# Performance work log

Measured on AMD Instinct MI355X. Metric: run time of the kernel, lower is better.

Reference implementation:

```python
import jax, jax.numpy as jnp
import numpy as np

HIDDEN = 1024

def setup_inputs() -> dict:
    key = jax.random.key(0)
    ks = jax.random.split(key, 7)
    B, S, H = 4, 4096, HIDDEN
    x = jax.random.normal(ks[0], (B, S, H), dtype=jnp.float32)
    s = 1.0 / np.sqrt(H)
    Wq = jax.random.normal(ks[1], (H, H), dtype=jnp.float32) * s
    bq = jnp.zeros((H,), dtype=jnp.float32)
    Wk = jax.random.normal(ks[2], (H, H), dtype=jnp.float32) * s
    bk = jnp.zeros((H,), dtype=jnp.float32)
    Wv = jax.random.normal(ks[3], (H, H), dtype=jnp.float32) * s
    bv = jnp.zeros((H,), dtype=jnp.float32)
    return {"x": x, "Wq": Wq, "bq": bq, "Wk": Wk, "bk": bk, "Wv": Wv, "bv": bv}

def reference(x, Wq, bq, Wk, bk, Wv, bv):
    # x: [B, S, H]
    scale = jnp.sqrt(jnp.asarray(x.shape[-1], dtype=x.dtype))
    q = jnp.einsum('bsh,hd->bsd', x, Wq) + bq
    k = jnp.einsum('bsh,hd->bsd', x, Wk) + bk
    v = jnp.einsum('bsh,hd->bsd', x, Wv) + bv
    energy = jnp.einsum('bqd,bkd->bqk', q, k) / scale  # [B, S, S]
    attn = jax.nn.softmax(energy, axis=-1)
    return jnp.einsum('bqk,bkd->bqd', attn, v)
```

## Files before the change

### kernel.cpp

```cpp
#include <hip/hip_runtime.h>

typedef unsigned short u16;
typedef __attribute__((ext_vector_type(8))) short short8;
typedef __attribute__((ext_vector_type(4))) short short4v;
typedef __attribute__((ext_vector_type(4))) float floatx4;

#define HD 1024
#define SEQ 4096

__device__ inline u16 f2bf(float f) {
    union { float f; unsigned int i; } c; c.f = f;
    unsigned int r = c.i + 0x7fffu + ((c.i >> 16) & 1u);
    return (u16)(r >> 16);
}

__device__ inline float bf2f(u16 h) {
    union { unsigned int u; float f; } c; c.u = ((unsigned int)h) << 16;
    return c.f;
}

__device__ inline int xcd_chunk(int bid, int nwg) {
    int q = nwg >> 3;
    return (bid & 7) * q + (bid >> 3);
}

__device__ inline void glds16(const u16* g, u16* l) {
    __builtin_amdgcn_global_load_lds(
        (const __attribute__((address_space(1))) unsigned int*)(const void*)g,
        (__attribute__((address_space(3))) unsigned int*)(void*)l, 16, 0, 0);
}

__global__ __launch_bounds__(256) void cvt_kernel(const float* __restrict__ in,
                                                  u16* __restrict__ out, int n4) {
    int idx = blockIdx.x * 256 + threadIdx.x;
    int stride = gridDim.x * 256;
    for (int i = idx; i < n4; i += stride) {
        floatx4 v = ((const floatx4*)in)[i];
        short4v o;
        o[0] = (short)f2bf(v[0]); o[1] = (short)f2bf(v[1]);
        o[2] = (short)f2bf(v[2]); o[3] = (short)f2bf(v[3]);
        ((short4v*)out)[i] = o;
    }
}

__global__ __launch_bounds__(256) void wt_kernel(const float* __restrict__ Wq,
                                                 const float* __restrict__ Wk,
                                                 const float* __restrict__ Wv,
                                                 u16* __restrict__ wt) {
    __shared__ u16 tile[64 * 65];
    int z = blockIdx.z;
    const float* W = (z == 0) ? Wq : ((z == 1) ? Wk : Wv);
    u16* out = wt + (size_t)z * HD * HD;
    int k0 = blockIdx.x * 64, n0 = blockIdx.y * 64;
    int t = threadIdx.x;
    int r = t >> 4, c4 = (t & 15) * 4;
    for (int h = 0; h < 4; ++h) {
        int row = r + h * 16;
        floatx4 v = *(const floatx4*)(W + (size_t)(k0 + row) * HD + n0 + c4);
        tile[row * 65 + c4 + 0] = f2bf(v[0]);
        tile[row * 65 + c4 + 1] = f2bf(v[1]);
        tile[row * 65 + c4 + 2] = f2bf(v[2]);
        tile[row * 65 + c4 + 3] = f2bf(v[3]);
    }
    __syncthreads();
    int r2 = t >> 3, c8 = (t & 7) * 8;
    union { short8 v; u16 u[8]; } buf;
    for (int h = 0; h < 2; ++h) {
        int rr = r2 + h * 32;
        #pragma unroll
        for (int i = 0; i < 8; ++i) buf.u[i] = tile[(c8 + i) * 65 + rr];
        *(short8*)(out + (size_t)(n0 + rr) * HD + k0 + c8) = buf.v;
    }
}

#define RD_A(i, ks) (*(const short8*)&As[(wm * 128 + (i) * 16 + l16) * 64 + ((((ks) * 4 + quad)) ^ (l16 & 7)) * 8])
#define RD_B(j, ks) (*(const short8*)&Bs[(wn * 64 + (j) * 16 + l16) * 64 + ((((ks) * 4 + quad)) ^ (l16 & 7)) * 8])

#define GEMM256_CORE(KTN, LDA_, LDB_)                                                   \
    int t = threadIdx.x, lane = t & 63, w = t >> 6;                                     \
    int quad = lane >> 4, l16 = lane & 15;                                              \
    int wm = w >> 2, wn = w & 3;                                                        \
    int l8r = lane >> 3;                                                                \
    int sswz = (lane & 7) ^ l8r;                                                        \
    const u16* gAs = Ab + (size_t)(m0 + w * 32 + l8r) * LDA_ + sswz * 8;                \
    const u16* gBs = Bb + (size_t)(n0 + w * 32 + l8r) * LDB_ + sswz * 8;                \
    auto stage = [&](int kt_) {                                                         \
        int s_ = kt_ & 1;                                                               \
        const u16* a0 = gAs + (size_t)kt_ * 64;                                         \
        const u16* b0 = gBs + (size_t)kt_ * 64;                                         \
        _Pragma("unroll")                                                               \
        for (int L = 0; L < 4; ++L) {                                                   \
            glds16(a0 + (size_t)(8 * L) * LDA_, &ring[s_][0][(w * 32 + 8 * L) * 64]);   \
            glds16(b0 + (size_t)(8 * L) * LDB_, &ring[s_][1][(w * 32 + 8 * L) * 64]);   \
        }                                                                               \
    };                                                                                  \
    floatx4 acc[8][4] = {};                                                             \
    stage(0);                                                                           \
    for (int kt = 0; kt < (KTN); ++kt) {                                                \
        asm volatile("s_waitcnt vmcnt(0)" ::: "memory");        \
        __builtin_amdgcn_s_barrier();                         \
        asm volatile("" ::: "memory");                                                  \
        if (kt + 1 < (KTN)) stage(kt + 1);      \
        const u16* As = &ring[kt & 1][0][0];                                            \
        const u16* Bs = &ring[kt & 1][1][0];                                            \
        short8 bfr[2][4];                                                               \
        short8 afr[2][2];                                                               \
        _Pragma("unroll")                                                               \
        for (int j = 0; j < 4; ++j) bfr[0][j] = RD_B(j, 0);                             \
        afr[0][0] = RD_A(0, 0);                                                         \
        afr[0][1] = RD_A(1, 0);                                                         \
        _Pragma("unroll")                                                               \
        for (int p = 0; p < 8; ++p) {                                                   \
            int ks = p >> 2, q = p & 3;                                                 \
            int cur = p & 1, nxt = cur ^ 1;                                             \
            if (p < 7) {                                                                \
                int pn = p + 1;                                                         \
                int ksn = pn >> 2, qn = pn & 3;                                         \
                if (qn == 0) {                                                          \
                    _Pragma("unroll")                                                   \
                    for (int j = 0; j < 4; ++j) bfr[1][j] = RD_B(j, 1);                 \
                }                                                                       \
                afr[nxt][0] = RD_A(2 * qn, ksn);                                        \
                afr[nxt][1] = RD_A(2 * qn + 1, ksn);                                    \
            }                                                                           \
            __builtin_amdgcn_s_setprio(1);                                              \
            _Pragma("unroll")                                                           \
            for (int j = 0; j < 4; ++j) {                                               \
                acc[2 * q][j] = __builtin_amdgcn_mfma_f32_16x16x32_bf16(afr[cur][0], bfr[ks][j], acc[2 * q][j], 0, 0, 0);       \
                acc[2 * q + 1][j] = __builtin_amdgcn_mfma_f32_16x16x32_bf16(afr[cur][1], bfr[ks][j], acc[2 * q + 1][j], 0, 0, 0); \
            }                                                                           \
            __builtin_amdgcn_s_setprio(0);                                              \
        }                                                                               \
    }

template<int LDA, int LDB, int LDC, int KT, int MT, int NT, bool F32OUT>
__global__ __launch_bounds__(512, 2) void gemm256(const u16* __restrict__ A,
                                                  const u16* __restrict__ B,
                                                  void* __restrict__ C,
                                                  float scale) {
    __shared__ __align__(16) u16 ring[2][2][256 * 64];
    constexpr int NWG = 4 * MT * NT;
    int wg = xcd_chunk(blockIdx.x, NWG);
    int b = wg / (MT * NT);
    int r = wg % (MT * NT);
    int m0 = (r / NT) * 256, n0 = (r % NT) * 256;
    const u16* Ab = A + (size_t)b * MT * 256 * LDA;
    const u16* Bb = B + (size_t)b * NT * 256 * LDB;

    GEMM256_CORE(KT, LDA, LDB)

    if constexpr (F32OUT) {
        float* Cb = (float*)C + (size_t)b * MT * 256 * LDC;
        #pragma unroll
        for (int i = 0; i < 8; ++i)
            #pragma unroll
            for (int rr = 0; rr < 4; ++rr) {
                int m = m0 + wm * 128 + i * 16 + quad * 4 + rr;
                float* row = Cb + (size_t)m * LDC + n0 + wn * 64 + l16;
                #pragma unroll
                for (int j = 0; j < 4; ++j)
                    row[j * 16] = acc[i][j][rr] * scale;
            }
    } else {
        u16* Cb = (u16*)C + (size_t)b * MT * 256 * LDC;
        #pragma unroll
        for (int i = 0; i < 8; ++i)
            #pragma unroll
            for (int rr = 0; rr < 4; ++rr) {
                int m = m0 + wm * 128 + i * 16 + quad * 4 + rr;
                u16* row = Cb + (size_t)m * LDC + n0 + wn * 64 + l16;
                #pragma unroll
                for (int j = 0; j < 4; ++j)
                    row[j * 16] = f2bf(acc[i][j][rr] * scale);
            }
    }
}

__global__ __launch_bounds__(512, 2) void qkv256(const u16* __restrict__ x,
                                                 const u16* __restrict__ wt,
                                                 const float* __restrict__ bq,
                                                 const float* __restrict__ bk,
                                                 u16* __restrict__ qb,
                                                 u16* __restrict__ kbuf) {
    __shared__ __align__(16) u16 ring[2][2][256 * 64];
    int wg = xcd_chunk(blockIdx.x, 512);
    int z = wg >> 8;
    int r = wg & 255;
    int m0 = (r >> 2) * 256, n0 = (r & 3) * 256;
    const u16* Ab = x;
    const u16* Bb = wt + (size_t)z * HD * HD;
    const float* bias = z ? bk : bq;
    u16* C = z ? kbuf : qb;

    GEMM256_CORE(16, HD, HD)

    float bb[4];
    #pragma unroll
    for (int j = 0; j < 4; ++j) bb[j] = bias[n0 + wn * 64 + j * 16 + l16];
    #pragma unroll
    for (int i = 0; i < 8; ++i)
        #pragma unroll
        for (int rr = 0; rr < 4; ++rr) {
            int m = m0 + wm * 128 + i * 16 + quad * 4 + rr;
            u16* row = C + (size_t)m * HD + n0 + wn * 64 + l16;
            #pragma unroll
            for (int j = 0; j < 4; ++j)
                row[j * 16] = f2bf(acc[i][j][rr] + bb[j]);
        }
}

__global__ __launch_bounds__(256, 2) void v_gemm(const u16* __restrict__ x,
                                                 const u16* __restrict__ wtv,
                                                 const float* __restrict__ bv,
                                                 u16* __restrict__ vtb) {
    __shared__ __align__(16) u16 sA[128 * 32];
    __shared__ __align__(16) u16 sB[128 * 32];
    __shared__ __align__(16) u16 tileC[128 * 132];
    int m0 = blockIdx.x * 128, n0 = blockIdx.y * 128;
    int t = threadIdx.x, lane = t & 63, w = t >> 6;
    int quad = lane >> 4, l16 = lane & 15;
    int wm = w >> 1, wn = w & 1;
    floatx4 acc[4][4] = {};

    int srow = w * 32 + (lane >> 2);
    int sswz = (lane & 3) ^ ((lane >> 3) & 3);
    const u16* gA = x + (size_t)(m0 + srow) * HD + sswz * 8;
    const u16* gB = wtv + (size_t)(n0 + srow) * HD + sswz * 8;
    u16* lA0 = &sA[(w * 32) * 32];
    u16* lA1 = &sA[(w * 32 + 16) * 32];
    u16* lB0 = &sB[(w * 32) * 32];
    u16* lB1 = &sB[(w * 32 + 16) * 32];

    for (int k0 = 0; k0 < HD; k0 += 32) {
        glds16(gA + k0, lA0);
        glds16(gA + (size_t)16 * HD + k0, lA1);
        glds16(gB + k0, lB0);
        glds16(gB + (size_t)16 * HD + k0, lB1);
        __syncthreads();
        short8 af[4], bfr[4];
        #pragma unroll
        for (int i = 0; i < 4; ++i) {
            int ra = wm * 64 + i * 16 + l16;
            af[i] = *(const short8*)&sA[ra * 32 + (quad ^ ((ra >> 1) & 3)) * 8];
        }
        #pragma unroll
        for (int j = 0; j < 4; ++j) {
            int rb = wn * 64 + j * 16 + l16;
            bfr[j] = *(const short8*)&sB[rb * 32 + (quad ^ ((rb >> 1) & 3)) * 8];
        }
        #pragma unroll
        for (int i = 0; i < 4; ++i)
            #pragma unroll
            for (int j = 0; j < 4; ++j)
                acc[i][j] = __builtin_amdgcn_mfma_f32_16x16x32_bf16(af[i], bfr[j], acc[i][j], 0, 0, 0);
        __syncthreads();
    }

    #pragma unroll
    for (int j = 0; j < 4; ++j) {
        int nl = wn * 64 + j * 16 + l16;
        float bb = bv[n0 + nl];
        #pragma unroll
        for (int i = 0; i < 4; ++i) {
            #pragma unroll
            for (int rr = 0; rr < 4; ++rr) {
                int ml = wm * 64 + i * 16 + quad * 4 + rr;
                tileC[ml * 132 + nl] = f2bf(acc[i][j][rr] + bb);
            }
        }
    }
    __syncthreads();
    int r = t >> 1, c0 = (t & 1) * 64;
    int b_ = m0 >> 12, s0 = m0 & 4095;
    #pragma unroll
    for (int v = 0; v < 8; ++v) {
        union { short8 vv; u16 u[8]; } pk;
        #pragma unroll
        for (int e = 0; e < 8; ++e) pk.u[e] = tileC[(c0 + v * 8 + e) * 132 + r];
        *(short8*)&vtb[((size_t)(b_ * HD + n0 + r)) * SEQ + s0 + c0 + v * 8] = pk.vv;
    }
}

__global__ __launch_bounds__(256, 2) void qkv_gemm(const u16* __restrict__ x,
                                                   const u16* __restrict__ wt,
                                                   const float* __restrict__ bq,
                                                   const float* __restrict__ bk,
                                                   const float* __restrict__ bv,
                                                   u16* __restrict__ qb,
                                                   u16* __restrict__ kbuf,
                                                   u16* __restrict__ vtb) {
    __shared__ __align__(16) u16 sA[128 * 32];
    __shared__ __align__(16) u16 sB[128 * 32];
    __shared__ __align__(16) u16 tileC[128 * 132];
    int z = blockIdx.z;
    const u16* Bt = wt + (size_t)z * HD * HD;
    const float* bias = (z == 0) ? bq : ((z == 1) ? bk : bv);
    int m0 = blockIdx.x * 128, n0 = blockIdx.y * 128;
    int t = threadIdx.x, lane = t & 63, w = t >> 6;
    int quad = lane >> 4, l16 = lane & 15;
    int wm = w >> 1, wn = w & 1;
    floatx4 acc[4][4] = {};

    int srow = w * 32 + (lane >> 2);
    int sswz = (lane & 3) ^ ((lane >> 3) & 3);
    const u16* gA = x + (size_t)(m0 + srow) * HD + sswz * 8;
    const u16* gB = Bt + (size_t)(n0 + srow) * HD + sswz * 8;
    u16* lA0 = &sA[(w * 32) * 32];
    u16* lA1 = &sA[(w * 32 + 16) * 32];
    u16* lB0 = &sB[(w * 32) * 32];
    u16* lB1 = &sB[(w * 32 + 16) * 32];

    for (int k0 = 0; k0 < HD; k0 += 32) {
        glds16(gA + k0, lA0);
        glds16(gA + (size_t)16 * HD + k0, lA1);
        glds16(gB + k0, lB0);
        glds16(gB + (size_t)16 * HD + k0, lB1);
        __syncthreads();
        short8 af[4], bfr[4];
        #pragma unroll
        for (int i = 0; i < 4; ++i) {
            int ra = wm * 64 + i * 16 + l16;
            af[i] = *(const short8*)&sA[ra * 32 + (quad ^ ((ra >> 1) & 3)) * 8];
        }
        #pragma unroll
        for (int j = 0; j < 4; ++j) {
            int rb = wn * 64 + j * 16 + l16;
            bfr[j] = *(const short8*)&sB[rb * 32 + (quad ^ ((rb >> 1) & 3)) * 8];
        }
        #pragma unroll
        for (int i = 0; i < 4; ++i)
            #pragma unroll
            for (int j = 0; j < 4; ++j)
                acc[i][j] = __builtin_amdgcn_mfma_f32_16x16x32_bf16(af[i], bfr[j], acc[i][j], 0, 0, 0);
        __syncthreads();
    }

    #pragma unroll
    for (int j = 0; j < 4; ++j) {
        int nl = wn * 64 + j * 16 + l16;
        float bb = bias[n0 + nl];
        #pragma unroll
        for (int i = 0; i < 4; ++i) {
            #pragma unroll
            for (int rr = 0; rr < 4; ++rr) {
                int ml = wm * 64 + i * 16 + quad * 4 + rr;
                tileC[ml * 132 + nl] = f2bf(acc[i][j][rr] + bb);
            }
        }
    }
    __syncthreads();
    int r = t >> 1, c0 = (t & 1) * 64;
    if (z != 2) {
        u16* dst = (z == 0) ? qb : kbuf;
        #pragma unroll
        for (int v = 0; v < 8; ++v) {
            short8 vv = *(const short8*)&tileC[r * 132 + c0 + v * 8];
            *(short8*)&dst[(size_t)(m0 + r) * HD + n0 + c0 + v * 8] = vv;
        }
    } else {
        int b_ = m0 >> 12, s0 = m0 & 4095;
        #pragma unroll
        for (int v = 0; v < 8; ++v) {
            union { short8 vv; u16 u[8]; } pk;
            #pragma unroll
            for (int e = 0; e < 8; ++e) pk.u[e] = tileC[(c0 + v * 8 + e) * 132 + r];
            *(short8*)&vtb[((size_t)(b_ * HD + n0 + r)) * SEQ + s0 + c0 + v * 8] = pk.vv;
        }
    }
}

__global__ __launch_bounds__(256) void softmax_kernel(u16* __restrict__ S) {
    int w = threadIdx.x >> 6, lane = threadIdx.x & 63;
    size_t row = (size_t)blockIdx.x * 4 + w;
    u16* p = S + row * SEQ;
    float sv[64];
    float mx = -1e30f;
    #pragma unroll
    for (int c = 0; c < 8; ++c) {
        short8 v = *(const short8*)&p[(c * 64 + lane) * 8];
        #pragma unroll
        for (int e = 0; e < 8; ++e) {
            float f = bf2f((u16)v[e]);
            sv[c * 8 + e] = f;
            mx = fmaxf(mx, f);
        }
    }
    mx = fmaxf(mx, __shfl_xor(mx, 1));
    mx = fmaxf(mx, __shfl_xor(mx, 2));
    mx = fmaxf(mx, __shfl_xor(mx, 4));
    mx = fmaxf(mx, __shfl_xor(mx, 8));
    mx = fmaxf(mx, __shfl_xor(mx, 16));
    mx = fmaxf(mx, __shfl_xor(mx, 32));
    float sum = 0.f;
    #pragma unroll
    for (int i = 0; i < 64; ++i) { sv[i] = __expf(sv[i] - mx); sum += sv[i]; }
    sum += __shfl_xor(sum, 1);
    sum += __shfl_xor(sum, 2);
    sum += __shfl_xor(sum, 4);
    sum += __shfl_xor(sum, 8);
    sum += __shfl_xor(sum, 16);
    sum += __shfl_xor(sum, 32);
    float rinv = 1.f / sum;
    #pragma unroll
    for (int c = 0; c < 8; ++c) {
        union { short8 vv; u16 u[8]; } o;
        #pragma unroll
        for (int e = 0; e < 8; ++e) o.u[e] = f2bf(sv[c * 8 + e] * rinv);
        *(short8*)&p[(c * 64 + lane) * 8] = o.vv;
    }
}

__global__ __launch_bounds__(512, 2) void flash_kernel(const u16* __restrict__ q,
                                                       const u16* __restrict__ k,
                                                       const u16* __restrict__ vt,
                                                       float* __restrict__ out) {
    __shared__ __align__(16) u16 q_lds[64 * 1032];
    __shared__ float Sc[64 * 66];
    __shared__ __align__(16) u16 Pb[64 * 72];
    __shared__ float m_st[64], l_st[64], al_st[64];

    int t = threadIdx.x, lane = t & 63, w = t >> 6;
    int quad = lane >> 4, l16 = lane & 15;
    int j = w & 3, hh = w >> 2;
    int bid = blockIdx.x;
    int xcd = bid & 7;
    int b = xcd >> 1;
    int q0 = (((bid >> 3) << 1) + (xcd & 1)) * 64;

    for (int i = t; i < 64 * 128; i += 512) {
        int r = i >> 7, c8 = (i & 127) * 8;
        *(short8*)&q_lds[r * 1032 + c8] =
            *(const short8*)&q[((size_t)(b * SEQ + q0 + r)) * HD + c8];
    }
    if (t < 64) { m_st[t] = -1e30f; l_st[t] = 0.f; }
    floatx4 o_acc[4][8] = {};
    __syncthreads();

    const u16* kwave = k + ((size_t)(b * SEQ + j * 16 + l16)) * HD + hh * 512 + quad * 8;
    const u16* vwave = vt + ((size_t)(b * HD + w * 128 + l16)) * SEQ + quad * 8;
    int r2 = t >> 3;
    int cg = (t & 7) * 8;

    for (int tt = 0; tt < 64; ++tt) {
        int kb = tt * 64;
        floatx4 s_acc[4] = {};
        const u16* kp = kwave + (size_t)kb * HD;
        #pragma unroll 8
        for (int ks = 0; ks < 16; ++ks) {
            short8 kf = *(const short8*)(kp + ks * 32);
            #pragma unroll
            for (int rb = 0; rb < 4; ++rb) {
                short8 qf = *(const short8*)&q_lds[(rb * 16 + l16) * 1032 + hh * 512 + ks * 32 + quad * 8];
                s_acc[rb] = __builtin_amdgcn_mfma_f32_16x16x32_bf16(qf, kf, s_acc[rb], 0, 0, 0);
            }
        }
        if (hh == 0) {
            #pragma unroll
            for (int rb = 0; rb < 4; ++rb)
                #pragma unroll
                for (int rr = 0; rr < 4; ++rr)
                    Sc[(rb * 16 + quad * 4 + rr) * 66 + j * 16 + l16] = s_acc[rb][rr] * 0.03125f;
        }
        __syncthreads();
        if (hh == 1) {
            #pragma unroll
            for (int rb = 0; rb < 4; ++rb)
                #pragma unroll
                for (int rr = 0; rr < 4; ++rr)
                    Sc[(rb * 16 + quad * 4 + rr) * 66 + j * 16 + l16] += s_acc[rb][rr] * 0.03125f;
        }
        __syncthreads();

        float sv[8];
        float mloc = -1e30f;
        #pragma unroll
        for (int i = 0; i < 8; ++i) { sv[i] = Sc[r2 * 66 + cg + i]; mloc = fmaxf(mloc, sv[i]); }
        mloc = fmaxf(mloc, __shfl_xor(mloc, 1));
        mloc = fmaxf(mloc, __shfl_xor(mloc, 2));
        mloc = fmaxf(mloc, __shfl_xor(mloc, 4));
        float m_old = m_st[r2];
        float m_new = fmaxf(m_old, mloc);
        float alpha = __expf(m_old - m_new);
        float sum = 0.f;
        #pragma unroll
        for (int i = 0; i < 8; ++i) {
            float p = __expf(sv[i] - m_new);
            sum += p;
            Pb[r2 * 72 + cg + i] = f2bf(p);
        }
        sum += __shfl_xor(sum, 1);
        sum += __shfl_xor(sum, 2);
        sum += __shfl_xor(sum, 4);
        if ((t & 7) == 0) {
            m_st[r2] = m_new;
            l_st[r2] = l_st[r2] * alpha + sum;
            al_st[r2] = alpha;
        }
        __syncthreads();

        #pragma unroll
        for (int rb = 0; rb < 4; ++rb) {
            float a0 = al_st[rb * 16 + quad * 4 + 0];
            float a1 = al_st[rb * 16 + quad * 4 + 1];
            float a2 = al_st[rb * 16 + quad * 4 + 2];
            float a3 = al_st[rb * 16 + quad * 4 + 3];
            #pragma unroll
            for (int dt = 0; dt < 8; ++dt) {
                o_acc[rb][dt][0] *= a0;
                o_acc[rb][dt][1] *= a1;
                o_acc[rb][dt][2] *= a2;
                o_acc[rb][dt][3] *= a3;
            }
        }
        short8 pf[4][2];
        #pragma unroll
        for (int rb = 0; rb < 4; ++rb)
            #pragma unroll
            for (int ks2 = 0; ks2 < 2; ++ks2)
                pf[rb][ks2] = *(const short8*)&Pb[(rb * 16 + l16) * 72 + ks2 * 32 + quad * 8];
        const u16* vp = vwave + kb;
        #pragma unroll
        for (int dt = 0; dt < 8; ++dt) {
            short8 vf0 = *(const short8*)(vp + (size_t)dt * 16 * SEQ);
            short8 vf1 = *(const short8*)(vp + (size_t)dt * 16 * SEQ + 32);
            #pragma unroll
            for (int rb = 0; rb < 4; ++rb) {
                o_acc[rb][dt] = __builtin_amdgcn_mfma_f32_16x16x32_bf16(pf[rb][0], vf0, o_acc[rb][dt], 0, 0, 0);
                o_acc[rb][dt] = __builtin_amdgcn_mfma_f32_16x16x32_bf16(pf[rb][1], vf1, o_acc[rb][dt], 0, 0, 0);
            }
        }
    }

    #pragma unroll
    for (int rb = 0; rb < 4; ++rb) {
        #pragma unroll
        for (int rr = 0; rr < 4; ++rr) {
            int row = rb * 16 + quad * 4 + rr;
            float linv = 1.f / l_st[row];
            #pragma unroll
            for (int dt = 0; dt < 8; ++dt) {
                out[((size_t)(b * SEQ + q0 + row)) * HD + w * 128 + dt * 16 + l16] =
                    o_acc[rb][dt][rr] * linv;
            }
        }
    }
}

extern "C" void kernel_launch(void* const* d_in, const int* in_sizes, int n_in,
                              void* d_out, int out_size, void* d_ws, size_t ws_size,
                              hipStream_t stream) {
    const float* x  = (const float*)d_in[0];
    const float* Wq = (const float*)d_in[1];
    const float* bq = (const float*)d_in[2];
    const float* Wk = (const float*)d_in[3];
    const float* bk = (const float*)d_in[4];
    const float* Wv = (const float*)d_in[5];
    const float* bv = (const float*)d_in[6];
    float* out = (float*)d_out;
    char* ws = (char*)d_ws;
    const size_t MB = 1024 * 1024;

    if (ws_size >= 224 * MB) {
        u16* vtb = (u16*)ws;
        u16* qb  = (u16*)(ws + 32 * MB);
        u16* kb  = (u16*)(ws + 64 * MB);
        u16* S   = (u16*)(ws + 96 * MB);
        u16* xb  = (u16*)(ws + 96 * MB);
        u16* wt  = (u16*)(ws + 128 * MB);

        cvt_kernel<<<dim3(4096), 256, 0, stream>>>(x, xb, (4 * SEQ * HD) / 4);
        wt_kernel<<<dim3(16, 16, 3), 256, 0, stream>>>(Wq, Wk, Wv, wt);
        qkv256<<<dim3(512), 512, 0, stream>>>(xb, wt, bq, bk, qb, kb);
        v_gemm<<<dim3(128, 8), 256, 0, stream>>>(xb, wt + (size_t)2 * HD * HD, bv, vtb);
        gemm256<HD, HD, SEQ, 16, 16, 16, false><<<dim3(1024), 512, 0, stream>>>(qb, kb, S, 0.03125f);
        softmax_kernel<<<dim3(4096), 256, 0, stream>>>(S);
        gemm256<SEQ, SEQ, HD, 64, 16, 4, true><<<dim3(256), 512, 0, stream>>>(S, vtb, out, 1.0f);
    } else {
        u16* xb  = (u16*)ws;
        u16* wt  = (u16*)(ws + 32 * MB);
        u16* qb  = (u16*)(ws + 38 * MB);
        u16* kb  = (u16*)(ws + 70 * MB);
        u16* vtb = (u16*)(ws + 102 * MB);

        cvt_kernel<<<dim3(4096), 256, 0, stream>>>(x, xb, (4 * SEQ * HD) / 4);
        wt_kernel<<<dim3(16, 16, 3), 256, 0, stream>>>(Wq, Wk, Wv, wt);
        qkv_gemm<<<dim3(128, 8, 3), 256, 0, stream>>>(xb, wt, bq, bk, bv, qb, kb, vtb);
        flash_kernel<<<dim3(256), 512, 0, stream>>>(qb, kb, vtb, out);
    }
}
```

Before: 504.9 us.

## Restructure GEMM inner loop into four MFMA phases with extra workgroup barriers

Replaces the 8-step software-pipelined LDS-read/MFMA loop with four phases. All B fragments for both k-steps are loaded up front, and A fragments are loaded in double-buffered pairs ahead of each 16-MFMA block. Workgroup barriers are added between phases so the waves stay in lockstep and their LDS reads interleave with MFMA issue. This trades extra barriers and higher register pressure for more regular overlap of LDS reads with matrix math.

```diff
diff --git a/kernel.cpp b/kernel.cpp
--- a/kernel.cpp
+++ b/kernel.cpp
@@ -75,6 +75,18 @@
 
 #define RD_A(i, ks) (*(const short8*)&As[(wm * 128 + (i) * 16 + l16) * 64 + ((((ks) * 4 + quad)) ^ (l16 & 7)) * 8])
 #define RD_B(j, ks) (*(const short8*)&Bs[(wn * 64 + (j) * 16 + l16) * 64 + ((((ks) * 4 + quad)) ^ (l16 & 7)) * 8])
+
+#define MFMA16(F0, F1, I0, I1)                                                          \
+    __builtin_amdgcn_s_setprio(1);                                                      \
+    _Pragma("unroll")                                                                   \
+    for (int ks = 0; ks < 2; ++ks) {                                                    \
+        _Pragma("unroll")                                                               \
+        for (int j = 0; j < 4; ++j) {                                                   \
+            acc[I0][j] = __builtin_amdgcn_mfma_f32_16x16x32_bf16(F0[ks], bfr[j][ks], acc[I0][j], 0, 0, 0); \
+            acc[I1][j] = __builtin_amdgcn_mfma_f32_16x16x32_bf16(F1[ks], bfr[j][ks], acc[I1][j], 0, 0, 0); \
+        }                                                                               \
+    }                                                                                   \
+    __builtin_amdgcn_s_setprio(0);
 
 #define GEMM256_CORE(KTN, LDA_, LDB_)                                                   \
     int t = threadIdx.x, lane = t & 63, w = t >> 6;                                     \
@@ -103,34 +115,26 @@
         if (kt + 1 < (KTN)) stage(kt + 1);      \
         const u16* As = &ring[kt & 1][0][0];                                            \
         const u16* Bs = &ring[kt & 1][1][0];                                            \
-        short8 bfr[2][4];                                                               \
-        short8 afr[2][2];                                                               \
+        short8 bfr[4][2];                                                               \
         _Pragma("unroll")                                                               \
-        for (int j = 0; j < 4; ++j) bfr[0][j] = RD_B(j, 0);                             \
-        afr[0][0] = RD_A(0, 0);                                                         \
-        afr[0][1] = RD_A(1, 0);                                                         \
-        _Pragma("unroll")                                                               \
-        for (int p = 0; p < 8; ++p) {                                                   \
-            int ks = p >> 2, q = p & 3;                                                 \
-            int cur = p & 1, nxt = cur ^ 1;                                             \
-            if (p < 7) {                                                                \
-                int pn = p + 1;                                                         \
-                int ksn = pn >> 2, qn = pn & 3;                                         \
-                if (qn == 0) {                                                          \
-                    _Pragma("unroll")                                                   \
-                    for (int j = 0; j < 4; ++j) bfr[1][j] = RD_B(j, 1);                 \
-                }                                                                       \
-                afr[nxt][0] = RD_A(2 * qn, ksn);                                        \
-                afr[nxt][1] = RD_A(2 * qn + 1, ksn);                                    \
-            }                                                                           \
-            __builtin_amdgcn_s_setprio(1);                                              \
-            _Pragma("unroll")                                                           \
-            for (int j = 0; j < 4; ++j) {                                               \
-                acc[2 * q][j] = __builtin_amdgcn_mfma_f32_16x16x32_bf16(afr[cur][0], bfr[ks][j], acc[2 * q][j], 0, 0, 0);       \
-                acc[2 * q + 1][j] = __builtin_amdgcn_mfma_f32_16x16x32_bf16(afr[cur][1], bfr[ks][j], acc[2 * q + 1][j], 0, 0, 0); \
-            }                                                                           \
-            __builtin_amdgcn_s_setprio(0);                                              \
-        }                                                                               \
+        for (int j = 0; j < 4; ++j) { bfr[j][0] = RD_B(j, 0); bfr[j][1] = RD_B(j, 1); } \
+        short8 a0_[2], a1_[2], b0_[2], b1_[2];                                          \
+        a0_[0] = RD_A(0, 0); a0_[1] = RD_A(0, 1);                                       \
+        a1_[0] = RD_A(1, 0); a1_[1] = RD_A(1, 1);                                       \
+        b0_[0] = RD_A(2, 0); b0_[1] = RD_A(2, 1);                                       \
+        b1_[0] = RD_A(3, 0); b1_[1] = RD_A(3, 1);                                       \
+        __builtin_amdgcn_s_barrier();                              \
+        MFMA16(a0_, a1_, 0, 1)                                                          \
+        a0_[0] = RD_A(4, 0); a0_[1] = RD_A(4, 1);                                       \
+        a1_[0] = RD_A(5, 0); a1_[1] = RD_A(5, 1);                                       \
+        __builtin_amdgcn_s_barrier();          \
+        MFMA16(b0_, b1_, 2, 3)                                                          \
+        b0_[0] = RD_A(6, 0); b0_[1] = RD_A(6, 1);                                       \
+        b1_[0] = RD_A(7, 0); b1_[1] = RD_A(7, 1);                                       \
+        __builtin_amdgcn_s_barrier();                              \
+        MFMA16(a0_, a1_, 4, 5)                                                          \
+        __builtin_amdgcn_s_barrier();                              \
+        MFMA16(b0_, b1_, 6, 7)                                                          \
     }
 
 template<int LDA, int LDB, int LDC, int KT, int MT, int NT, bool F32OUT>
```

After: 527.3 us. 4.4% more time.
